# Optimization experiments

Hardware: AMD Instinct MI355X
Metric: run time of the kernel (lower is better)

The kernel has to match this reference:

```python
import jax, jax.numpy as jnp
import numpy as np
import math

SI, VI = 128, 32
H_DIM = 32          # max(vi, vo) for q/k/v GVPs; max(vi, 0)=32 for weight_proj
HEADS = 4
N_ANCHORS = 32
S_H, V_H = SI // HEADS, VI // HEADS  # 32, 8


def _norm_no_nan(x, axis=-1, keepdims=False, eps=1e-8):
    return jnp.sqrt(jnp.maximum(jnp.sum(x * x, axis=axis, keepdims=keepdims), eps))


def _gvp_full(s, v, wh, ws_w, ws_b, wv, wsv_w, wsv_b):
    # GVP with activations=(silu, sigmoid), vector_gate=True, vo>0
    vt = jnp.swapaxes(v, -1, -2)                 # [..., 3, vi]
    vh = vt @ wh.T                               # [..., 3, h]
    vn = _norm_no_nan(vh, axis=-2)               # [..., h]
    s_out = jnp.concatenate([s, vn], -1) @ ws_w.T + ws_b   # [..., so]
    v_out = jnp.swapaxes(vh @ wv.T, -1, -2)      # [..., vo, 3]
    gate = jax.nn.sigmoid(s_out) @ wsv_w.T + wsv_b
    v_out = v_out * jax.nn.sigmoid(gate)[..., None]
    return jax.nn.silu(s_out), v_out


def _gvp_scalar(s, v, wh, ws_w, ws_b):
    # weight_proj: activations=(None, None), vo=0 -> scalar output only
    vt = jnp.swapaxes(v, -1, -2)
    vh = vt @ wh.T
    vn = _norm_no_nan(vh, axis=-2)
    return jnp.concatenate([s, vn], -1) @ ws_w.T + ws_b


def setup_inputs() -> dict:
    key = jax.random.key(0)
    ks = jax.random.split(key, 32)
    N, C = 8192, 16
    inp = {
        's': jax.random.normal(ks[0], (N, C, SI), jnp.float32),
        'v': jax.random.normal(ks[1], (N, C, VI, 3), jnp.float32),
    }

    def lin(k, out_d, in_d):
        return jax.random.normal(k, (out_d, in_d), jnp.float32) / math.sqrt(in_d)

    # weight_proj: GVP((128,32) -> (32,0)), h_dim = max(32,0) = 32
    inp['wp_wh'] = lin(ks[2], H_DIM, VI)
    inp['wp_ws_w'] = lin(ks[3], N_ANCHORS, H_DIM + SI)
    inp['wp_ws_b'] = jnp.zeros((N_ANCHORS,), jnp.float32)
    # to_q / to_k / to_v: GVP((128,32) -> (128,32)), h_dim = 32
    i = 4
    for p in ('q', 'k', 'vp'):
        inp[f'{p}_wh'] = lin(ks[i], H_DIM, VI); i += 1
        inp[f'{p}_ws_w'] = lin(ks[i], SI, H_DIM + SI); i += 1
        inp[f'{p}_ws_b'] = jnp.zeros((SI,), jnp.float32)
        inp[f'{p}_wv'] = lin(ks[i], VI, H_DIM); i += 1
        inp[f'{p}_wsv_w'] = lin(ks[i], VI, SI); i += 1
        inp[f'{p}_wsv_b'] = jnp.zeros((VI,), jnp.float32)
    return inp


def reference(s, v, wp_wh, wp_ws_w, wp_ws_b,
              q_wh, q_ws_w, q_ws_b, q_wv, q_wsv_w, q_wsv_b,
              k_wh, k_ws_w, k_ws_b, k_wv, k_wsv_w, k_wsv_b,
              vp_wh, vp_ws_w, vp_ws_b, vp_wv, vp_wsv_w, vp_wsv_b):
    N, C = s.shape[:2]
    H, r = HEADS, N_ANCHORS

    # Compress: softmax over nodes -> r anchors
    p_logits = _gvp_scalar(s, v, wp_wh, wp_ws_w, wp_ws_b)       # [N, C, r]
    p_weights = jax.nn.softmax(p_logits, axis=0)
    s_global = jnp.einsum('nca,ncs->acs', p_weights, s)          # [r, C, si]
    v_global = jnp.einsum('nca,ncvd->acvd', p_weights, v)        # [r, C, vi, 3]

    s_q, v_q = _gvp_full(s, v, q_wh, q_ws_w, q_ws_b, q_wv, q_wsv_w, q_wsv_b)
    s_k, v_k = _gvp_full(s_global, v_global, k_wh, k_ws_w, k_ws_b, k_wv, k_wsv_w, k_wsv_b)
    s_val, v_val = _gvp_full(s_global, v_global, vp_wh, vp_ws_w, vp_ws_b, vp_wv, vp_wsv_w, vp_wsv_b)

    # split heads
    qs = s_q.reshape(N, C, H, S_H); qv = v_q.reshape(N, C, H, V_H, 3)
    ks_ = s_k.reshape(r, C, H, S_H); kv = v_k.reshape(r, C, H, V_H, 3)
    vs = s_val.reshape(r, C, H, S_H); vv = v_val.reshape(r, C, H, V_H, 3)

    s_dot = jnp.einsum('nchs,rchs->nrch', qs, ks_)
    v_dot = jnp.einsum('nchvd,rchvd->nrch', qv, kv)
    energy = (s_dot + v_dot) / math.sqrt(S_H + V_H)
    alpha = jax.nn.softmax(energy, axis=1)                       # softmax over anchors r
    # dropout is identity at inference

    out_s = jnp.einsum('nrch,rchs->nchs', alpha, vs).reshape(N, C, SI)
    out_v = jnp.einsum('nrch,rchvd->nchvd', alpha, vv).reshape(N, C, VI, 3)
    return out_s, out_v
```

## Files before the change

kernel.cpp:

```cpp
#include <hip/hip_runtime.h>
#include <stdint.h>

typedef unsigned short ushort_t;
typedef __attribute__((ext_vector_type(8))) short short8;
typedef __attribute__((ext_vector_type(4))) float float4v;

static constexpr int N_=8192, C_=16;

static constexpr long OFF_LOGITS = 0;
static constexpr long OFF_PM  = 4194304;
static constexpr long OFF_PS  = 4210688;
static constexpr long OFF_M   = 4227072;
static constexpr long OFF_INV = 4227584;
static constexpr long OFF_SGL = 4228096;
static constexpr long OFF_VGL = 4293632;
static constexpr long OFF_KATT= 4342784;
static constexpr long OFF_VATT= 4408320;
static constexpr long OFF_WF  = 4473856;
static constexpr long WF_WHQ=0, WF_WHWP=1024, WF_KWH=2048, WF_KWS=3072, WF_KWV=23552,
  WF_KWSV=24576, WF_VWH=28672, WF_VWS=29696, WF_VWV=50176, WF_VWSV=51200,
  WF_B1=55296 , WF_BG=70656 ,
  WF_BV=72704 ;

static constexpr long VH_B   = 67108864;
static constexpr long AVN_B  = 92274688;
static constexpr long PART_B = 67108864;
static constexpr long PART_ROWSZ = 224;
static constexpr long PART_CHUNKSZ = 512*224;

__device__ __forceinline__ uint32_t f2bf(float f){
  uint32_t u = __float_as_uint(f);
  return (u + 0x7FFFu + ((u>>16)&1u)) >> 16;
}

__device__ __forceinline__ void split_bf(float f, short& hi, short& lo){
  uint32_t u = __float_as_uint(f);
  uint32_t h = (u + 0x7FFFu + ((u>>16)&1u)) >> 16;
  hi = (short)h;
  float fh = __uint_as_float(h << 16);
  float r = f - fh;
  uint32_t u2 = __float_as_uint(r);
  lo = (short)((u2 + 0x7FFFu + ((u2>>16)&1u)) >> 16);
}

__device__ __forceinline__ long katt_idx(int c, int h, int k, int r){
  int kt=k>>5, kk=k&31, nt=r>>4;
  int lane=((kk>>3)<<4)|(r&15), j=kk&7;
  return ((((long)(c*4+h)*2+kt)*2+nt)*64+lane)*8+j;
}
__device__ __forceinline__ long vatt_idx(int c, int h, int r, int n2){
  int nt=n2>>4;
  int lane=((r>>3)<<4)|(n2&15), j=r&7;
  return (((long)(c*4+h)*4+nt)*64+lane)*8+j;
}

__global__ void k0_prep(const float* __restrict__ wpwh, const float* __restrict__ wpws,
    const float* __restrict__ qwh, const float* __restrict__ qws, const float* __restrict__ qwv,
    const float* __restrict__ qwsv, const float* __restrict__ kwh, const float* __restrict__ kws,
    const float* __restrict__ kwv, const float* __restrict__ kwsv, const float* __restrict__ vwh,
    const float* __restrict__ vws, const float* __restrict__ vwv, const float* __restrict__ vwsv,
    float* __restrict__ wsf){
  int job=blockIdx.x, t=threadIdx.x;
  float* W = wsf + OFF_WF;
  auto tr=[&](const float* src, float* dst, int O, int J){
    for(int idx=t; idx<O*J; idx+=blockDim.x){int o=idx/J, j=idx-o*J; dst[j*O+o]=src[idx];}
  };
  switch(job){
    case 0: tr(qwh,  W+WF_WHQ, 32,32); break;
    case 1: tr(wpwh, W+WF_WHWP,32,32); break;
    case 2: tr(kwh,  W+WF_KWH, 32,32); break;
    case 3: tr(kws,  W+WF_KWS, 128,160); break;
    case 4: tr(kwv,  W+WF_KWV, 32,32); break;
    case 5: tr(kwsv, W+WF_KWSV,32,128); break;
    case 6: tr(vwh,  W+WF_VWH, 32,32); break;
    case 7: tr(vws,  W+WF_VWS, 128,160); break;
    case 8: tr(vwv,  W+WF_VWV, 32,32); break;
    case 9: tr(vwsv, W+WF_VWSV,32,128); break;
    case 10: {
      ushort_t* dst=(ushort_t*)(W+WF_B1);
      for(int idx=t; idx<30720; idx+=blockDim.x){
        int j=idx&7, lane=(idx>>3)&63, tn=idx>>9, nt=tn%10, kt=tn/10;
        int k=kt*32+((lane>>4)<<3)+j, n=nt*16+(lane&15);
        float val;
        if(k<128)       val = (n<128)? qws[n*160+k]            : wpws[(n-128)*160+k];
        else if(k<160)  val = (n<128)? qws[n*160+k]            : 0.f;
        else            val = (n<128)? 0.f                     : wpws[(n-128)*160+(k-32)];
        dst[idx]=(ushort_t)f2bf(val);
      } } break;
    case 11: {
      ushort_t* dst=(ushort_t*)(W+WF_BG);
      for(int idx=t; idx<4096; idx+=blockDim.x){
        int j=idx&7, lane=(idx>>3)&63, tn=idx>>9, nt=tn&1, kt=tn>>1;
        int k=kt*32+((lane>>4)<<3)+j, n=nt*16+(lane&15);
        dst[idx]=(ushort_t)f2bf(qwsv[n*128+k]);
      } } break;
    case 12: {
      ushort_t* dst=(ushort_t*)(W+WF_BV);
      for(int idx=t; idx<1024; idx+=blockDim.x){
        int j=idx&7, lane=(idx>>3)&63, nt=idx>>9;
        int k=((lane>>4)<<3)+j, n=nt*16+(lane&15);
        dst[idx]=(ushort_t)f2bf(qwv[n*32+k]);
      } } break;
  }
}

__global__ __launch_bounds__(256) void kA_vn(const float* __restrict__ v,
    const float* __restrict__ wsf, ushort_t* __restrict__ vh_s, ushort_t* __restrict__ avn_s){
  __shared__ float whq[1024], whwp[1024];
  __shared__ float vb[4][96];
  int t=threadIdx.x, wave=t>>6, lane=t&63;
  for(int i=t;i<1024;i+=256){ whq[i]=wsf[OFF_WF+WF_WHQ+i]; whwp[i]=wsf[OFF_WF+WF_WHWP+i]; }
  __syncthreads();
  int h=lane&31, half=lane>>5;
  for(int it=0; it<32; it++){
    long inst = ((long)blockIdx.x*4 + wave)*32 + it;
    if(lane<48) ((float2*)vb[wave])[lane] = ((const float2*)v)[inst*48+lane];
    float d0=0,d1=0,d2=0;
    for(int i=half*16;i<half*16+16;i++){ float w=whq[i*32+h];
      d0+=vb[wave][3*i]*w; d1+=vb[wave][3*i+1]*w; d2+=vb[wave][3*i+2]*w; }
    d0+=__shfl_xor(d0,32,64); d1+=__shfl_xor(d1,32,64); d2+=__shfl_xor(d2,32,64);
    if(lane<32){
      float vn=sqrtf(fmaxf(d0*d0+d1*d1+d2*d2,1e-8f));
      avn_s[inst*64+h]=(ushort_t)f2bf(vn);
      vh_s[(inst*3+0)*32+h]=(ushort_t)f2bf(d0);
      vh_s[(inst*3+1)*32+h]=(ushort_t)f2bf(d1);
      vh_s[(inst*3+2)*32+h]=(ushort_t)f2bf(d2);
    }
    float e0=0,e1=0,e2=0;
    for(int i=half*16;i<half*16+16;i++){ float w=whwp[i*32+h];
      e0+=vb[wave][3*i]*w; e1+=vb[wave][3*i+1]*w; e2+=vb[wave][3*i+2]*w; }
    e0+=__shfl_xor(e0,32,64); e1+=__shfl_xor(e1,32,64); e2+=__shfl_xor(e2,32,64);
    if(lane<32){
      float vn=sqrtf(fmaxf(e0*e0+e1*e1+e2*e2,1e-8f));
      avn_s[inst*64+32+h]=(ushort_t)f2bf(vn);
    }
  }
}

__global__ __launch_bounds__(256) void kB_gemm(const float* __restrict__ s,
    float* __restrict__ wsf,
    const float* __restrict__ qwsb, const float* __restrict__ wpwsb,
    const float* __restrict__ qwsvb,
    ushort_t* __restrict__ qatt, const ushort_t* __restrict__ vh_s,
    const ushort_t* __restrict__ avn_s){
  __shared__ ushort_t sigl[4][16*136];
  __shared__ float    gsigl[4][16*33];
  int t=threadIdx.x, wave=t>>6, lane=t&63;
  int l15=lane&15, lq=lane>>4;
  long m0 = ((long)blockIdx.x*4 + wave)*16;
  const short8* B1 = (const short8*)(wsf + OFF_WF + WF_B1);
  const short8* BG = (const short8*)(wsf + OFF_WF + WF_BG);
  const short8* BV = (const short8*)(wsf + OFF_WF + WF_BV);
  float4v acc[10];
  #pragma unroll
  for(int i=0;i<10;i++) acc[i]=(float4v){0.f,0.f,0.f,0.f};
  #pragma unroll
  for(int kt=0;kt<4;kt++){
    const float* sp = s + (m0+l15)*128 + kt*32 + lq*8;
    float4 f0=*(const float4*)sp, f1=*(const float4*)(sp+4);
    short8 a;
    a[0]=(short)f2bf(f0.x); a[1]=(short)f2bf(f0.y); a[2]=(short)f2bf(f0.z); a[3]=(short)f2bf(f0.w);
    a[4]=(short)f2bf(f1.x); a[5]=(short)f2bf(f1.y); a[6]=(short)f2bf(f1.z); a[7]=(short)f2bf(f1.w);
    #pragma unroll
    for(int nt=0;nt<10;nt++)
      acc[nt]=__builtin_amdgcn_mfma_f32_16x16x32_bf16(a, B1[(kt*10+nt)*64+lane], acc[nt],0,0,0);
  }
  #pragma unroll
  for(int kt=4;kt<6;kt++){
    short8 a = *(const short8*)&avn_s[(m0+l15)*64 + (kt-4)*32 + lq*8];
    #pragma unroll
    for(int nt=0;nt<10;nt++)
      acc[nt]=__builtin_amdgcn_mfma_f32_16x16x32_bf16(a, B1[(kt*10+nt)*64+lane], acc[nt],0,0,0);
  }
  ushort_t* sl = sigl[wave]; float* gl = gsigl[wave];
  #pragma unroll
  for(int nt=0;nt<8;nt++){
    float b = qwsb[nt*16+l15];
    #pragma unroll
    for(int reg=0;reg<4;reg++){
      float x = acc[nt][reg] + b;
      float sg = 1.f/(1.f+__expf(-x));
      int row = lq*4+reg, col=nt*16+l15;
      long inst = m0+row;
      qatt[(inst*4 + (col>>5))*64 + (col&31)] = (ushort_t)f2bf(x*sg);
      sl[row*136+col] = (ushort_t)f2bf(sg);
    }
  }
  #pragma unroll
  for(int nt=8;nt<10;nt++){
    float b = wpwsb[(nt-8)*16+l15];
    #pragma unroll
    for(int reg=0;reg<4;reg++){
      long inst=m0+lq*4+reg;
      wsf[OFF_LOGITS + inst*32 + (nt-8)*16+l15] = acc[nt][reg]+b;
    }
  }
  __syncthreads();
  float4v g0=(float4v){0.f,0.f,0.f,0.f}, g1=g0;
  #pragma unroll
  for(int kt=0;kt<4;kt++){
    short8 a = *(const short8*)&sl[l15*136 + kt*32 + lq*8];
    g0=__builtin_amdgcn_mfma_f32_16x16x32_bf16(a, BG[(kt*2+0)*64+lane], g0,0,0,0);
    g1=__builtin_amdgcn_mfma_f32_16x16x32_bf16(a, BG[(kt*2+1)*64+lane], g1,0,0,0);
  }
  {
    float b0 = qwsvb[l15], b1 = qwsvb[16+l15];
    #pragma unroll
    for(int reg=0;reg<4;reg++){
      int row=lq*4+reg;
      gl[row*33 + l15]    = 1.f/(1.f+__expf(-(g0[reg]+b0)));
      gl[row*33 + 16+l15] = 1.f/(1.f+__expf(-(g1[reg]+b1)));
    }
  }
  __syncthreads();
  #pragma unroll
  for(int tt=0;tt<3;tt++){
    short8 a = *(const short8*)&vh_s[(m0*3 + tt*16 + l15)*32 + lq*8];
    float4v v0=(float4v){0.f,0.f,0.f,0.f}, v1=v0;
    v0=__builtin_amdgcn_mfma_f32_16x16x32_bf16(a, BV[0*64+lane], v0,0,0,0);
    v1=__builtin_amdgcn_mfma_f32_16x16x32_bf16(a, BV[1*64+lane], v1,0,0,0);
    #pragma unroll
    for(int nt2=0;nt2<2;nt2++){
      #pragma unroll
      for(int reg=0;reg<4;reg++){
        int lr = tt*16 + lq*4 + reg;
        int il = lr/3, d = lr - il*3;
        int o = nt2*16+l15;
        float val = (nt2? v1[reg] : v0[reg]) * gl[il*33+o];
        long inst = m0 + il;
        qatt[(inst*4 + (o>>3))*64 + 32 + (o&7)*3 + d] = (ushort_t)f2bf(val);
      }
    }
  }
}

__global__ __launch_bounds__(256) void k2a_stats(float* __restrict__ ws){
  int c = blockIdx.x; int chunk = blockIdx.y;
  int t=threadIdx.x; int i=t>>5, a=t&31;
  const float* L = ws + OFF_LOGITS;
  float m=-1e30f, sum=0.f;
  for(int k2=0;k2<32;k2++){
    int n = chunk*256 + k2*8 + i;
    float x = L[((long)n*16 + c)*32 + a];
    float mn = fmaxf(m,x);
    sum = sum*__expf(m-mn) + __expf(x-mn);
    m = mn;
  }
  __shared__ float sm[8][32], ss[8][32];
  sm[i][a]=m; ss[i][a]=sum;
  __syncthreads();
  if(t<32){
    float M=sm[0][t], S=ss[0][t];
    for(int q=1;q<8;q++){
      float mq=sm[q][t], sq_=ss[q][t];
      float mn=fmaxf(M,mq); S=S*__expf(M-mn)+sq_*__expf(mq-mn); M=mn;
    }
    ws[OFF_PM + (chunk*16+c)*32 + t]=M;
    ws[OFF_PS + (chunk*16+c)*32 + t]=S;
  }
}

__global__ __launch_bounds__(256) void k2b_merge(float* __restrict__ ws){
  int t = blockIdx.x*256 + threadIdx.x;
  if(t>=512) return;
  int c=t>>5, a=t&31;
  float M=-1e30f, S=0.f;
  for(int ch=0; ch<32; ch++){
    float mq=ws[OFF_PM+(ch*16+c)*32+a], sq_=ws[OFF_PS+(ch*16+c)*32+a];
    float mn=fmaxf(M,mq); S=S*__expf(M-mn)+sq_*__expf(mq-mn); M=mn;
  }
  ws[OFF_M + t]=M; ws[OFF_INV + t]=1.0f/S;
}

template<int NMT, bool ISV>
__device__ __forceinline__ void k3_body(const float* __restrict__ X, int dx0, int pb0,
    const float* __restrict__ L, float M0, float M1, float I0, float I1,
    int c, int nb0, int l15, int lq, float* __restrict__ partc){
  constexpr int XP = ISV ? 96 : 128;
  float4v acc[NMT][2];
  #pragma unroll
  for(int mi=0;mi<NMT;mi++){
    acc[mi][0]=(float4v){0.f,0.f,0.f,0.f};
    acc[mi][1]=(float4v){0.f,0.f,0.f,0.f};
  }
  #pragma unroll
  for(int kt=0;kt<4;kt++){
    int nb = nb0 + kt*32 + lq*8;
    short8 bh0, bl0, bh1, bl1;
    #pragma unroll
    for(int j=0;j<8;j++){
      long ro = ((long)(nb+j)*16 + c)*32;
      float w0 = __expf(L[ro + l15]      - M0) * I0;
      float w1 = __expf(L[ro + 16 + l15] - M1) * I1;
      short h_, lo_;
      split_bf(w0, h_, lo_); bh0[j]=h_; bl0[j]=lo_;
      split_bf(w1, h_, lo_); bh1[j]=h_; bl1[j]=lo_;
    }
    #pragma unroll
    for(int mi=0;mi<NMT;mi++){
      short8 ah, al_;
      #pragma unroll
      for(int j=0;j<8;j++){
        float f = X[((long)(nb+j)*16 + c)*XP + dx0 + mi*16 + l15];
        short h_, lo_;
        split_bf(f, h_, lo_); ah[j]=h_; al_[j]=lo_;
      }
      acc[mi][0]=__builtin_amdgcn_mfma_f32_16x16x32_bf16(ah,  bh0, acc[mi][0],0,0,0);
      acc[mi][0]=__builtin_amdgcn_mfma_f32_16x16x32_bf16(al_, bh0, acc[mi][0],0,0,0);
      acc[mi][0]=__builtin_amdgcn_mfma_f32_16x16x32_bf16(ah,  bl0, acc[mi][0],0,0,0);
      acc[mi][1]=__builtin_amdgcn_mfma_f32_16x16x32_bf16(ah,  bh1, acc[mi][1],0,0,0);
      acc[mi][1]=__builtin_amdgcn_mfma_f32_16x16x32_bf16(al_, bh1, acc[mi][1],0,0,0);
      acc[mi][1]=__builtin_amdgcn_mfma_f32_16x16x32_bf16(ah,  bl1, acc[mi][1],0,0,0);
    }
  }
  #pragma unroll
  for(int mi=0;mi<NMT;mi++){
    #pragma unroll
    for(int nt=0;nt<2;nt++){
      int a = nt*16 + l15;
      long row = (long)(a*16 + c);
      float4 val = make_float4(acc[mi][nt][0], acc[mi][nt][1], acc[mi][nt][2], acc[mi][nt][3]);
      *(float4*)&partc[row*PART_ROWSZ + pb0 + mi*16 + lq*4] = val;
    }
  }
}

__global__ __launch_bounds__(256) void k3_globals(const float* __restrict__ s,
    const float* __restrict__ v, const float* __restrict__ ws, float* __restrict__ part){
  int c = blockIdx.x & 15; int chunk = blockIdx.x >> 4;
  int t=threadIdx.x, wave=t>>6, lane=t&63;
  int l15=lane&15, lq=lane>>4;
  const float* L = ws + OFF_LOGITS;
  float M0 = ws[OFF_M   + c*32 + l15],      M1 = ws[OFF_M   + c*32 + 16 + l15];
  float I0 = ws[OFF_INV + c*32 + l15],      I1 = ws[OFF_INV + c*32 + 16 + l15];
  int nb0 = chunk*128;
  float* partc = part + (long)chunk*PART_CHUNKSZ;
  if(wave==0)      k3_body<4,false>(s, 0,  0,   L, M0,M1,I0,I1, c, nb0, l15, lq, partc);
  else if(wave==1) k3_body<4,false>(s, 64, 64,  L, M0,M1,I0,I1, c, nb0, l15, lq, partc);
  else if(wave==2) k3_body<3,true >(v, 0,  128, L, M0,M1,I0,I1, c, nb0, l15, lq, partc);
  else             k3_body<3,true >(v, 48, 176, L, M0,M1,I0,I1, c, nb0, l15, lq, partc);
}

__global__ __launch_bounds__(256) void k3r_reduce(const float* __restrict__ part,
    float* __restrict__ ws){
  int idx = blockIdx.x*256 + threadIdx.x;
  int ac = idx / 224, d = idx - ac*224;
  float sum = 0.f;
  #pragma unroll 8
  for(int ch=0; ch<64; ch++) sum += part[(long)ch*PART_CHUNKSZ + idx];
  if(d<128) ws[OFF_SGL + (long)ac*128 + d]       = sum;
  else      ws[OFF_VGL + (long)ac*96  + (d-128)] = sum;
}

__global__ __launch_bounds__(64) void k4_kvgvp(float* __restrict__ wsf,
    const float* __restrict__ k_wsb, const float* __restrict__ k_wsvb,
    const float* __restrict__ v_wsb, const float* __restrict__ v_wsvb){
  int a = blockIdx.x >> 4, c = blockIdx.x & 15;
  int lane = threadIdx.x;
  __shared__ __align__(16) float cat[160];
  __shared__ __align__(16) float vb2[96];
  __shared__ float vhb[96];
  __shared__ __align__(16) float sg[128];
  const float* W = wsf + OFF_WF;
  ushort_t* katt = (ushort_t*)(wsf + OFF_KATT);
  ushort_t* vatt = (ushort_t*)(wsf + OFF_VATT);
  long inst = (long)a*16 + c;
  ((float2*)cat)[lane] = ((const float2*)(wsf+OFF_SGL))[inst*64 + lane];
  if(lane<48) ((float2*)vb2)[lane] = ((const float2*)(wsf+OFF_VGL))[inst*48 + lane];
  __syncthreads();
  if(a==0){
    for(int idx=lane; idx<1024; idx+=64){
      int h2=idx&3, kk=56+((idx>>2)&7), r=idx>>5;
      katt[katt_idx(c,h2,kk,r)]=0;
      vatt[vatt_idx(c,h2,r,kk)]=0;
    }
  }
  int h = lane&31, half = lane>>5;
  for(int p=0;p<2;p++){
    const float* wht  = W + (p? WF_VWH  : WF_KWH);
    const float* wst  = W + (p? WF_VWS  : WF_KWS);
    const float* wvt  = W + (p? WF_VWV  : WF_KWV);
    const float* wsvt = W + (p? WF_VWSV : WF_KWSV);
    const float* bs   = p? v_wsb : k_wsb;
    const float* bsv  = p? v_wsvb : k_wsvb;
    float d0=0.f,d1=0.f,d2=0.f;
    for(int i=half*16; i<half*16+16; i++){
      float w_=wht[i*32+h];
      d0+=vb2[3*i]*w_; d1+=vb2[3*i+1]*w_; d2+=vb2[3*i+2]*w_;
    }
    d0 += __shfl_xor(d0,32,64); d1 += __shfl_xor(d1,32,64); d2 += __shfl_xor(d2,32,64);
    if(lane<32){
      cat[128+h] = sqrtf(fmaxf(d0*d0+d1*d1+d2*d2, 1e-8f));
      vhb[3*h]=d0; vhb[3*h+1]=d1; vhb[3*h+2]=d2;
    }
    __syncthreads();
    float a0=bs[lane], a1=bs[lane+64];
    for(int j=0;j<160;j+=4){
      float4 c4=*((float4*)&cat[j]);
      a0 += c4.x*wst[j*128+lane]      + c4.y*wst[(j+1)*128+lane]
          + c4.z*wst[(j+2)*128+lane]  + c4.w*wst[(j+3)*128+lane];
      a1 += c4.x*wst[j*128+64+lane]   + c4.y*wst[(j+1)*128+64+lane]
          + c4.z*wst[(j+2)*128+64+lane]+ c4.w*wst[(j+3)*128+64+lane];
    }
    float sig0=1.f/(1.f+__expf(-a0)), sig1=1.f/(1.f+__expf(-a1));
    float silu0=a0*sig0, silu1=a1*sig1;
    sg[lane]=sig0; sg[lane+64]=sig1;
    {
      int o=lane, hh2=o>>5, k=o&31;
      if(p==0) katt[katt_idx(c,hh2,k,a)] = (ushort_t)f2bf(silu0);
      else     vatt[vatt_idx(c,hh2,a,k)] = (ushort_t)f2bf(silu0);
    }
    {
      int o=lane+64, hh2=o>>5, k=o&31;
      if(p==0) katt[katt_idx(c,hh2,k,a)] = (ushort_t)f2bf(silu1);
      else     vatt[vatt_idx(c,hh2,a,k)] = (ushort_t)f2bf(silu1);
    }
    __syncthreads();
    float gacc=0.f;
    for(int o=half*64; o<half*64+64; o+=4){
      float4 s4_=*((float4*)&sg[o]);
      gacc += s4_.x*wsvt[o*32+h]+s4_.y*wsvt[(o+1)*32+h]+s4_.z*wsvt[(o+2)*32+h]+s4_.w*wsvt[(o+3)*32+h];
    }
    gacc += __shfl_xor(gacc,32,64);
    float sgate = 1.f/(1.f+__expf(-(gacc + bsv[h])));
    float e0=0.f,e1=0.f,e2=0.f;
    for(int hh=half*16; hh<half*16+16; hh++){
      float w_=wvt[hh*32+h];
      e0+=vhb[3*hh]*w_; e1+=vhb[3*hh+1]*w_; e2+=vhb[3*hh+2]*w_;
    }
    e0+=__shfl_xor(e0,32,64); e1+=__shfl_xor(e1,32,64); e2+=__shfl_xor(e2,32,64);
    if(lane<32){
      int hh2=lane>>3, oo=lane&7;
      float vals[3]={e0*sgate, e1*sgate, e2*sgate};
      #pragma unroll
      for(int d=0;d<3;d++){
        if(p==0) katt[katt_idx(c,hh2,32+oo*3+d,a)] = (ushort_t)f2bf(vals[d]);
        else     vatt[vatt_idx(c,hh2,a,32+oo*3+d)] = (ushort_t)f2bf(vals[d]);
      }
    }
    __syncthreads();
  }
}

__global__ __launch_bounds__(256) void k5_attn(const float* __restrict__ wsf, float* out){
  __shared__ ushort_t al[4][4*16*40];
  int t=threadIdx.x, wave=t>>6, lane=t&63;
  int l15=lane&15, lq=lane>>4;
  int c=blockIdx.y;
  long n0 = ((long)blockIdx.x*4+wave)*16;
  const ushort_t* qatt = (const ushort_t*)out;
  const short8* KA = (const short8*)(wsf + OFF_KATT);
  const short8* VA = (const short8*)(wsf + OFF_VATT);
  const float scale = 0.15811388300841897f;
  float4v e[4][2];
  #pragma unroll
  for(int h=0;h<4;h++){ e[h][0]=(float4v){0.f,0.f,0.f,0.f}; e[h][1]=e[h][0]; }
  #pragma unroll
  for(int h=0;h<4;h++){
    #pragma unroll
    for(int kt=0;kt<2;kt++){
      short8 a = *(const short8*)&qatt[(((n0+l15)*16 + c)*4 + h)*64 + kt*32 + lq*8];
      e[h][0]=__builtin_amdgcn_mfma_f32_16x16x32_bf16(a, KA[(((c*4+h)*2+kt)*2+0)*64+lane], e[h][0],0,0,0);
      e[h][1]=__builtin_amdgcn_mfma_f32_16x16x32_bf16(a, KA[(((c*4+h)*2+kt)*2+1)*64+lane], e[h][1],0,0,0);
    }
  }
  ushort_t* alw = al[wave];
  #pragma unroll
  for(int h=0;h<4;h++){
    #pragma unroll
    for(int reg=0;reg<4;reg++){
      float a0=e[h][0][reg]*scale, a1=e[h][1][reg]*scale;
      float m=fmaxf(a0,a1);
      m=fmaxf(m,__shfl_xor(m,1,64)); m=fmaxf(m,__shfl_xor(m,2,64));
      m=fmaxf(m,__shfl_xor(m,4,64)); m=fmaxf(m,__shfl_xor(m,8,64));
      float p0=__expf(a0-m), p1=__expf(a1-m);
      float sum=p0+p1;
      sum+=__shfl_xor(sum,1,64); sum+=__shfl_xor(sum,2,64);
      sum+=__shfl_xor(sum,4,64); sum+=__shfl_xor(sum,8,64);
      float inv=1.f/sum;
      int row=lq*4+reg;
      alw[h*640 + row*40 + l15]      = (ushort_t)f2bf(p0*inv);
      alw[h*640 + row*40 + 16 + l15] = (ushort_t)f2bf(p1*inv);
    }
  }
  __syncthreads();
  float* outv = out + 16777216;
  #pragma unroll
  for(int h=0;h<4;h++){
    short8 a = *(const short8*)&alw[h*640 + l15*40 + lq*8];
    #pragma unroll
    for(int nt=0;nt<4;nt++){
      float4v o_=(float4v){0.f,0.f,0.f,0.f};
      o_=__builtin_amdgcn_mfma_f32_16x16x32_bf16(a, VA[((c*4+h)*4+nt)*64+lane], o_,0,0,0);
      #pragma unroll
      for(int reg=0;reg<4;reg++){
        int n2=nt*16+l15, row=lq*4+reg;
        long inst=(n0+row)*16+c;
        float val=o_[reg];
        if(n2<32)      out[inst*128 + h*32+n2]=val;
        else if(n2<56) outv[inst*96 + h*24 + n2-32]=val;
      }
    }
  }
}

extern "C" void kernel_launch(void* const* d_in, const int* in_sizes, int n_in,
                              void* d_out, int out_size, void* d_ws, size_t ws_size,
                              hipStream_t stream){
  (void)in_sizes; (void)n_in; (void)out_size; (void)ws_size;
  const float* s = (const float*)d_in[0];
  const float* v = (const float*)d_in[1];
  float* wsf = (float*)d_ws;
  float* out = (float*)d_out;
  ushort_t* qatt  = (ushort_t*)d_out;
  ushort_t* vh_s  = (ushort_t*)((char*)d_out + VH_B);
  ushort_t* avn_s = (ushort_t*)((char*)d_out + AVN_B);
  float* part = (float*)((char*)d_out + PART_B);
  k0_prep<<<13,256,0,stream>>>(
      (const float*)d_in[2],(const float*)d_in[3],
      (const float*)d_in[5],(const float*)d_in[6],(const float*)d_in[8],(const float*)d_in[9],
      (const float*)d_in[11],(const float*)d_in[12],(const float*)d_in[14],(const float*)d_in[15],
      (const float*)d_in[17],(const float*)d_in[18],(const float*)d_in[20],(const float*)d_in[21], wsf);
  kA_vn<<<1024,256,0,stream>>>(v, wsf, vh_s, avn_s);
  kB_gemm<<<2048,256,0,stream>>>(s, wsf, (const float*)d_in[7], (const float*)d_in[4],
                                 (const float*)d_in[10], qatt, vh_s, avn_s);
  k2a_stats<<<dim3(16,32),256,0,stream>>>(wsf);
  k2b_merge<<<2,256,0,stream>>>(wsf);
  k3_globals<<<1024,256,0,stream>>>(s, v, wsf, part);
  k3r_reduce<<<448,256,0,stream>>>(part, wsf);
  k4_kvgvp<<<512,64,0,stream>>>(wsf, (const float*)d_in[13], (const float*)d_in[16],
                                (const float*)d_in[19], (const float*)d_in[22]);
  k5_attn<<<dim3(128,16),256,0,stream>>>(wsf, out);
}
```

Baseline: 499.1 us.

## Fuse partial-sum reduction into k/v GVP kernel and hoist loads in gemm

Removes the separate k3r_reduce launch and has k4_kvgvp sum the 64 chunk partials directly into its shared buffers with float4 loads. In kB_gemm, all global loads (s, avn, vh) are issued up front, before the MFMA chain, so their latency overlaps. Block-wide __syncthreads that only guarded per-wave shared buffers are dropped in kB_gemm and k5_attn. The risk is that removing those barriers relies on each wave touching only its own LDS region, and the fused reduction puts more global reads into each 64-thread k4 block.

```diff
diff --git a/kernel.cpp b/kernel.cpp
--- a/kernel.cpp
+++ b/kernel.cpp
@@ -151,26 +151,39 @@
   const short8* B1 = (const short8*)(wsf + OFF_WF + WF_B1);
   const short8* BG = (const short8*)(wsf + OFF_WF + WF_BG);
   const short8* BV = (const short8*)(wsf + OFF_WF + WF_BV);
-  float4v acc[10];
-  #pragma unroll
-  for(int i=0;i<10;i++) acc[i]=(float4v){0.f,0.f,0.f,0.f};
+
+  float4 f[4][2];
   #pragma unroll
   for(int kt=0;kt<4;kt++){
     const float* sp = s + (m0+l15)*128 + kt*32 + lq*8;
-    float4 f0=*(const float4*)sp, f1=*(const float4*)(sp+4);
+    f[kt][0]=*(const float4*)sp; f[kt][1]=*(const float4*)(sp+4);
+  }
+  short8 A4 = *(const short8*)&avn_s[(m0+l15)*64 + lq*8];
+  short8 A5 = *(const short8*)&avn_s[(m0+l15)*64 + 32 + lq*8];
+  short8 av0 = *(const short8*)&vh_s[(m0*3 + 0*16 + l15)*32 + lq*8];
+  short8 av1 = *(const short8*)&vh_s[(m0*3 + 1*16 + l15)*32 + lq*8];
+  short8 av2 = *(const short8*)&vh_s[(m0*3 + 2*16 + l15)*32 + lq*8];
+
+  short8 A[6];
+  #pragma unroll
+  for(int kt=0;kt<4;kt++){
     short8 a;
-    a[0]=(short)f2bf(f0.x); a[1]=(short)f2bf(f0.y); a[2]=(short)f2bf(f0.z); a[3]=(short)f2bf(f0.w);
-    a[4]=(short)f2bf(f1.x); a[5]=(short)f2bf(f1.y); a[6]=(short)f2bf(f1.z); a[7]=(short)f2bf(f1.w);
+    a[0]=(short)f2bf(f[kt][0].x); a[1]=(short)f2bf(f[kt][0].y);
+    a[2]=(short)f2bf(f[kt][0].z); a[3]=(short)f2bf(f[kt][0].w);
+    a[4]=(short)f2bf(f[kt][1].x); a[5]=(short)f2bf(f[kt][1].y);
+    a[6]=(short)f2bf(f[kt][1].z); a[7]=(short)f2bf(f[kt][1].w);
+    A[kt]=a;
+  }
+  A[4]=A4; A[5]=A5;
+
+  float4v acc[10];
+  #pragma unroll
+  for(int i=0;i<10;i++) acc[i]=(float4v){0.f,0.f,0.f,0.f};
+  #pragma unroll
+  for(int kt=0;kt<6;kt++){
     #pragma unroll
     for(int nt=0;nt<10;nt++)
-      acc[nt]=__builtin_amdgcn_mfma_f32_16x16x32_bf16(a, B1[(kt*10+nt)*64+lane], acc[nt],0,0,0);
-  }
-  #pragma unroll
-  for(int kt=4;kt<6;kt++){
-    short8 a = *(const short8*)&avn_s[(m0+l15)*64 + (kt-4)*32 + lq*8];
-    #pragma unroll
-    for(int nt=0;nt<10;nt++)
-      acc[nt]=__builtin_amdgcn_mfma_f32_16x16x32_bf16(a, B1[(kt*10+nt)*64+lane], acc[nt],0,0,0);
+      acc[nt]=__builtin_amdgcn_mfma_f32_16x16x32_bf16(A[kt], B1[(kt*10+nt)*64+lane], acc[nt],0,0,0);
   }
   ushort_t* sl = sigl[wave]; float* gl = gsigl[wave];
   #pragma unroll
@@ -195,7 +208,6 @@
       wsf[OFF_LOGITS + inst*32 + (nt-8)*16+l15] = acc[nt][reg]+b;
     }
   }
-  __syncthreads();
   float4v g0=(float4v){0.f,0.f,0.f,0.f}, g1=g0;
   #pragma unroll
   for(int kt=0;kt<4;kt++){
@@ -212,10 +224,9 @@
       gl[row*33 + 16+l15] = 1.f/(1.f+__expf(-(g1[reg]+b1)));
     }
   }
-  __syncthreads();
   #pragma unroll
   for(int tt=0;tt<3;tt++){
-    short8 a = *(const short8*)&vh_s[(m0*3 + tt*16 + l15)*32 + lq*8];
+    short8 a = (tt==0)? av0 : (tt==1)? av1 : av2;
     float4v v0=(float4v){0.f,0.f,0.f,0.f}, v1=v0;
     v0=__builtin_amdgcn_mfma_f32_16x16x32_bf16(a, BV[0*64+lane], v0,0,0,0);
     v1=__builtin_amdgcn_mfma_f32_16x16x32_bf16(a, BV[1*64+lane], v1,0,0,0);
@@ -341,18 +352,8 @@
   else             k3_body<3,true >(v, 48, 176, L, M0,M1,I0,I1, c, nb0, l15, lq, partc);
 }
 
-__global__ __launch_bounds__(256) void k3r_reduce(const float* __restrict__ part,
-    float* __restrict__ ws){
-  int idx = blockIdx.x*256 + threadIdx.x;
-  int ac = idx / 224, d = idx - ac*224;
-  float sum = 0.f;
-  #pragma unroll 8
-  for(int ch=0; ch<64; ch++) sum += part[(long)ch*PART_CHUNKSZ + idx];
-  if(d<128) ws[OFF_SGL + (long)ac*128 + d]       = sum;
-  else      ws[OFF_VGL + (long)ac*96  + (d-128)] = sum;
-}
-
 __global__ __launch_bounds__(64) void k4_kvgvp(float* __restrict__ wsf,
+    const float* __restrict__ part,
     const float* __restrict__ k_wsb, const float* __restrict__ k_wsvb,
     const float* __restrict__ v_wsb, const float* __restrict__ v_wsvb){
   int a = blockIdx.x >> 4, c = blockIdx.x & 15;
@@ -364,9 +365,20 @@
   const float* W = wsf + OFF_WF;
   ushort_t* katt = (ushort_t*)(wsf + OFF_KATT);
   ushort_t* vatt = (ushort_t*)(wsf + OFF_VATT);
-  long inst = (long)a*16 + c;
-  ((float2*)cat)[lane] = ((const float2*)(wsf+OFF_SGL))[inst*64 + lane];
-  if(lane<48) ((float2*)vb2)[lane] = ((const float2*)(wsf+OFF_VGL))[inst*48 + lane];
+  long row = (long)a*16 + c;
+  {
+    float4 accp = make_float4(0.f,0.f,0.f,0.f);
+    if(lane<56){
+      const float* pp = part + row*PART_ROWSZ + lane*4;
+      #pragma unroll 8
+      for(int ch=0; ch<64; ch++){
+        float4 x = *(const float4*)(pp + (long)ch*PART_CHUNKSZ);
+        accp.x+=x.x; accp.y+=x.y; accp.z+=x.z; accp.w+=x.w;
+      }
+    }
+    if(lane<32)      *(float4*)&cat[lane*4]      = accp;
+    else if(lane<56) *(float4*)&vb2[(lane-32)*4] = accp;
+  }
   __syncthreads();
   if(a==0){
     for(int idx=lane; idx<1024; idx+=64){
@@ -483,7 +495,6 @@
       alw[h*640 + row*40 + 16 + l15] = (ushort_t)f2bf(p1*inv);
     }
   }
-  __syncthreads();
   float* outv = out + 16777216;
   #pragma unroll
   for(int h=0;h<4;h++){
@@ -527,8 +538,7 @@
   k2a_stats<<<dim3(16,32),256,0,stream>>>(wsf);
   k2b_merge<<<2,256,0,stream>>>(wsf);
   k3_globals<<<1024,256,0,stream>>>(s, v, wsf, part);
-  k3r_reduce<<<448,256,0,stream>>>(part, wsf);
-  k4_kvgvp<<<512,64,0,stream>>>(wsf, (const float*)d_in[13], (const float*)d_in[16],
+  k4_kvgvp<<<512,64,0,stream>>>(wsf, part, (const float*)d_in[13], (const float*)d_in[16],
                                 (const float*)d_in[19], (const float*)d_in[22]);
   k5_attn<<<dim3(128,16),256,0,stream>>>(wsf, out);
 }
```

Result: no change. 502.2 us (+0.6%).

## Fuse partial-sum reduction into k4 and run key/value GVPs in parallel waves

Applied to the files above, without the earlier changes.

Removes the separate k3r_reduce launch; k4 now sums the 64 chunk partials itself and uses two waves so the key and value GVPs run concurrently instead of looping. It also drops a __syncthreads in k5 (wave-private smem) and moves zeroing of qatt padding into kB_gemm. The aim is to save one kernel launch and serial latency in the small k4 stage. The reduction reads now happen inside k4's critical path, and PART_ROWSZ must match the earlier layout.

```diff
diff --git a/kernel.cpp b/kernel.cpp
--- a/kernel.cpp
+++ b/kernel.cpp
@@ -151,6 +151,10 @@
   const short8* B1 = (const short8*)(wsf + OFF_WF + WF_B1);
   const short8* BG = (const short8*)(wsf + OFF_WF + WF_BG);
   const short8* BV = (const short8*)(wsf + OFF_WF + WF_BV);
+  {
+    short8 z = {0,0,0,0,0,0,0,0};
+    *(short8*)&qatt[((m0+l15)*4 + lq)*64 + 56] = z;
+  }
   float4v acc[10];
   #pragma unroll
   for(int i=0;i<10;i++) acc[i]=(float4v){0.f,0.f,0.f,0.f};
@@ -341,104 +345,106 @@
   else             k3_body<3,true >(v, 48, 176, L, M0,M1,I0,I1, c, nb0, l15, lq, partc);
 }
 
-__global__ __launch_bounds__(256) void k3r_reduce(const float* __restrict__ part,
-    float* __restrict__ ws){
-  int idx = blockIdx.x*256 + threadIdx.x;
-  int ac = idx / 224, d = idx - ac*224;
-  float sum = 0.f;
-  #pragma unroll 8
-  for(int ch=0; ch<64; ch++) sum += part[(long)ch*PART_CHUNKSZ + idx];
-  if(d<128) ws[OFF_SGL + (long)ac*128 + d]       = sum;
-  else      ws[OFF_VGL + (long)ac*96  + (d-128)] = sum;
-}
-
-__global__ __launch_bounds__(64) void k4_kvgvp(float* __restrict__ wsf,
+__global__ __launch_bounds__(128) void k4_kvgvp(float* __restrict__ wsf,
+    const float* __restrict__ part,
     const float* __restrict__ k_wsb, const float* __restrict__ k_wsvb,
     const float* __restrict__ v_wsb, const float* __restrict__ v_wsvb){
   int a = blockIdx.x >> 4, c = blockIdx.x & 15;
-  int lane = threadIdx.x;
-  __shared__ __align__(16) float cat[160];
+  int t=threadIdx.x, p=t>>6, lane=t&63;
+  __shared__ __align__(16) float catw[2][160];
   __shared__ __align__(16) float vb2[96];
-  __shared__ float vhb[96];
-  __shared__ __align__(16) float sg[128];
+  __shared__ float vhb[2][96];
+  __shared__ __align__(16) float sg[2][128];
   const float* W = wsf + OFF_WF;
   ushort_t* katt = (ushort_t*)(wsf + OFF_KATT);
   ushort_t* vatt = (ushort_t*)(wsf + OFF_VATT);
-  long inst = (long)a*16 + c;
-  ((float2*)cat)[lane] = ((const float2*)(wsf+OFF_SGL))[inst*64 + lane];
-  if(lane<48) ((float2*)vb2)[lane] = ((const float2*)(wsf+OFF_VGL))[inst*48 + lane];
-  __syncthreads();
+  long row = (long)a*16 + c;
+  if(p==0){
+    float4 accp = make_float4(0.f,0.f,0.f,0.f);
+    if(lane<56){
+      const float* pp = part + row*PART_ROWSZ + lane*4;
+      #pragma unroll 8
+      for(int ch=0; ch<64; ch++){
+        float4 x = *(const float4*)(pp + (long)ch*PART_CHUNKSZ);
+        accp.x+=x.x; accp.y+=x.y; accp.z+=x.z; accp.w+=x.w;
+      }
+    }
+    if(lane<32)      *(float4*)&catw[0][lane*4]  = accp;
+    else if(lane<56) *(float4*)&vb2[(lane-32)*4] = accp;
+  }
   if(a==0){
-    for(int idx=lane; idx<1024; idx+=64){
+    for(int idx=t; idx<1024; idx+=128){
       int h2=idx&3, kk=56+((idx>>2)&7), r=idx>>5;
       katt[katt_idx(c,h2,kk,r)]=0;
       vatt[vatt_idx(c,h2,r,kk)]=0;
     }
   }
+  __syncthreads();
+  if(p==1 && lane<32) *(float4*)&catw[1][lane*4] = *(const float4*)&catw[0][lane*4];
+  const float* wht  = W + (p? WF_VWH  : WF_KWH);
+  const float* wst  = W + (p? WF_VWS  : WF_KWS);
+  const float* wvt  = W + (p? WF_VWV  : WF_KWV);
+  const float* wsvt = W + (p? WF_VWSV : WF_KWSV);
+  const float* bs   = p? v_wsb : k_wsb;
+  const float* bsv  = p? v_wsvb : k_wsvb;
+  float* cat = catw[p];
+  float* vh  = vhb[p];
+  float* sgp = sg[p];
   int h = lane&31, half = lane>>5;
-  for(int p=0;p<2;p++){
-    const float* wht  = W + (p? WF_VWH  : WF_KWH);
-    const float* wst  = W + (p? WF_VWS  : WF_KWS);
-    const float* wvt  = W + (p? WF_VWV  : WF_KWV);
-    const float* wsvt = W + (p? WF_VWSV : WF_KWSV);
-    const float* bs   = p? v_wsb : k_wsb;
-    const float* bsv  = p? v_wsvb : k_wsvb;
-    float d0=0.f,d1=0.f,d2=0.f;
-    for(int i=half*16; i<half*16+16; i++){
-      float w_=wht[i*32+h];
-      d0+=vb2[3*i]*w_; d1+=vb2[3*i+1]*w_; d2+=vb2[3*i+2]*w_;
-    }
-    d0 += __shfl_xor(d0,32,64); d1 += __shfl_xor(d1,32,64); d2 += __shfl_xor(d2,32,64);
-    if(lane<32){
-      cat[128+h] = sqrtf(fmaxf(d0*d0+d1*d1+d2*d2, 1e-8f));
-      vhb[3*h]=d0; vhb[3*h+1]=d1; vhb[3*h+2]=d2;
-    }
-    __syncthreads();
-    float a0=bs[lane], a1=bs[lane+64];
-    for(int j=0;j<160;j+=4){
-      float4 c4=*((float4*)&cat[j]);
-      a0 += c4.x*wst[j*128+lane]      + c4.y*wst[(j+1)*128+lane]
-          + c4.z*wst[(j+2)*128+lane]  + c4.w*wst[(j+3)*128+lane];
-      a1 += c4.x*wst[j*128+64+lane]   + c4.y*wst[(j+1)*128+64+lane]
-          + c4.z*wst[(j+2)*128+64+lane]+ c4.w*wst[(j+3)*128+64+lane];
-    }
-    float sig0=1.f/(1.f+__expf(-a0)), sig1=1.f/(1.f+__expf(-a1));
-    float silu0=a0*sig0, silu1=a1*sig1;
-    sg[lane]=sig0; sg[lane+64]=sig1;
-    {
-      int o=lane, hh2=o>>5, k=o&31;
-      if(p==0) katt[katt_idx(c,hh2,k,a)] = (ushort_t)f2bf(silu0);
-      else     vatt[vatt_idx(c,hh2,a,k)] = (ushort_t)f2bf(silu0);
-    }
-    {
-      int o=lane+64, hh2=o>>5, k=o&31;
-      if(p==0) katt[katt_idx(c,hh2,k,a)] = (ushort_t)f2bf(silu1);
-      else     vatt[vatt_idx(c,hh2,a,k)] = (ushort_t)f2bf(silu1);
-    }
-    __syncthreads();
-    float gacc=0.f;
-    for(int o=half*64; o<half*64+64; o+=4){
-      float4 s4_=*((float4*)&sg[o]);
-      gacc += s4_.x*wsvt[o*32+h]+s4_.y*wsvt[(o+1)*32+h]+s4_.z*wsvt[(o+2)*32+h]+s4_.w*wsvt[(o+3)*32+h];
-    }
-    gacc += __shfl_xor(gacc,32,64);
-    float sgate = 1.f/(1.f+__expf(-(gacc + bsv[h])));
-    float e0=0.f,e1=0.f,e2=0.f;
-    for(int hh=half*16; hh<half*16+16; hh++){
-      float w_=wvt[hh*32+h];
-      e0+=vhb[3*hh]*w_; e1+=vhb[3*hh+1]*w_; e2+=vhb[3*hh+2]*w_;
-    }
-    e0+=__shfl_xor(e0,32,64); e1+=__shfl_xor(e1,32,64); e2+=__shfl_xor(e2,32,64);
-    if(lane<32){
-      int hh2=lane>>3, oo=lane&7;
-      float vals[3]={e0*sgate, e1*sgate, e2*sgate};
-      #pragma unroll
-      for(int d=0;d<3;d++){
-        if(p==0) katt[katt_idx(c,hh2,32+oo*3+d,a)] = (ushort_t)f2bf(vals[d]);
-        else     vatt[vatt_idx(c,hh2,a,32+oo*3+d)] = (ushort_t)f2bf(vals[d]);
-      }
-    }
-    __syncthreads();
+  float d0=0.f,d1=0.f,d2=0.f;
+  for(int i=half*16; i<half*16+16; i++){
+    float w_=wht[i*32+h];
+    d0+=vb2[3*i]*w_; d1+=vb2[3*i+1]*w_; d2+=vb2[3*i+2]*w_;
+  }
+  d0 += __shfl_xor(d0,32,64); d1 += __shfl_xor(d1,32,64); d2 += __shfl_xor(d2,32,64);
+  if(lane<32){
+    cat[128+h] = sqrtf(fmaxf(d0*d0+d1*d1+d2*d2, 1e-8f));
+    vh[3*h]=d0; vh[3*h+1]=d1; vh[3*h+2]=d2;
+  }
+  __syncthreads();
+  float a0=bs[lane], a1=bs[lane+64];
+  for(int j=0;j<160;j+=4){
+    float4 c4=*((float4*)&cat[j]);
+    a0 += c4.x*wst[j*128+lane]      + c4.y*wst[(j+1)*128+lane]
+        + c4.z*wst[(j+2)*128+lane]  + c4.w*wst[(j+3)*128+lane];
+    a1 += c4.x*wst[j*128+64+lane]   + c4.y*wst[(j+1)*128+64+lane]
+        + c4.z*wst[(j+2)*128+64+lane]+ c4.w*wst[(j+3)*128+64+lane];
+  }
+  float sig0=1.f/(1.f+__expf(-a0)), sig1=1.f/(1.f+__expf(-a1));
+  float silu0=a0*sig0, silu1=a1*sig1;
+  sgp[lane]=sig0; sgp[lane+64]=sig1;
+  {
+    int o=lane, hh2=o>>5, k=o&31;
+    if(p==0) katt[katt_idx(c,hh2,k,a)] = (ushort_t)f2bf(silu0);
+    else     vatt[vatt_idx(c,hh2,a,k)] = (ushort_t)f2bf(silu0);
+  }
+  {
+    int o=lane+64, hh2=o>>5, k=o&31;
+    if(p==0) katt[katt_idx(c,hh2,k,a)] = (ushort_t)f2bf(silu1);
+    else     vatt[vatt_idx(c,hh2,a,k)] = (ushort_t)f2bf(silu1);
+  }
+  __syncthreads();
+  float gacc=0.f;
+  for(int o=half*64; o<half*64+64; o+=4){
+    float4 s4_=*((float4*)&sgp[o]);
+    gacc += s4_.x*wsvt[o*32+h]+s4_.y*wsvt[(o+1)*32+h]+s4_.z*wsvt[(o+2)*32+h]+s4_.w*wsvt[(o+3)*32+h];
+  }
+  gacc += __shfl_xor(gacc,32,64);
+  float sgate = 1.f/(1.f+__expf(-(gacc + bsv[h])));
+  float e0=0.f,e1=0.f,e2=0.f;
+  for(int hh=half*16; hh<half*16+16; hh++){
+    float w_=wvt[hh*32+h];
+    e0+=vh[3*hh]*w_; e1+=vh[3*hh+1]*w_; e2+=vh[3*hh+2]*w_;
+  }
+  e0+=__shfl_xor(e0,32,64); e1+=__shfl_xor(e1,32,64); e2+=__shfl_xor(e2,32,64);
+  if(lane<32){
+    int hh2=lane>>3, oo=lane&7;
+    float vals[3]={e0*sgate, e1*sgate, e2*sgate};
+    #pragma unroll
+    for(int d=0;d<3;d++){
+      if(p==0) katt[katt_idx(c,hh2,32+oo*3+d,a)] = (ushort_t)f2bf(vals[d]);
+      else     vatt[vatt_idx(c,hh2,a,32+oo*3+d)] = (ushort_t)f2bf(vals[d]);
+    }
   }
 }
 
@@ -483,7 +489,6 @@
       alw[h*640 + row*40 + 16 + l15] = (ushort_t)f2bf(p1*inv);
     }
   }
-  __syncthreads();
   float* outv = out + 16777216;
   #pragma unroll
   for(int h=0;h<4;h++){
@@ -527,8 +532,7 @@
   k2a_stats<<<dim3(16,32),256,0,stream>>>(wsf);
   k2b_merge<<<2,256,0,stream>>>(wsf);
   k3_globals<<<1024,256,0,stream>>>(s, v, wsf, part);
-  k3r_reduce<<<448,256,0,stream>>>(part, wsf);
-  k4_kvgvp<<<512,64,0,stream>>>(wsf, (const float*)d_in[13], (const float*)d_in[16],
-                                (const float*)d_in[19], (const float*)d_in[22]);
+  k4_kvgvp<<<512,128,0,stream>>>(wsf, part, (const float*)d_in[13], (const float*)d_in[16],
+                                 (const float*)d_in[19], (const float*)d_in[22]);
   k5_attn<<<dim3(128,16),256,0,stream>>>(wsf, out);
 }
```

New measurement: 504.0 us. No clear change (+1.0%).
